# Kernel optimization log

Measured on AMD Instinct MI355X. Metric: run time of the kernel, lower is better.

Reference implementation:

```python
import jax, jax.numpy as jnp
import numpy as np

N, M, D, E, G = 2048, 1024, 1024, 64, 16  # queries, keys, feat_dim, embed_dim, groups


def setup_inputs() -> dict:
    key = jax.random.key(0)
    ks = jax.random.split(key, 8)
    s = 0.02
    return {
        "ref_feat": jax.random.normal(ks[0], (N, D), jnp.float32),
        "sup_feat": jax.random.normal(ks[1], (M, D), jnp.float32),
        "position_embedding": jax.random.normal(ks[2], (1, E, N, M), jnp.float32),
        "fc_w": jax.random.normal(ks[3], (D, D), jnp.float32) * s,
        "fc_b": jnp.zeros((D,), jnp.float32),
        "wg_w": jax.random.normal(ks[4], (G, E, 1, 1), jnp.float32) * s,
        "wg_b": jnp.zeros((G,), jnp.float32),
        "wq_w": jax.random.normal(ks[5], (D, D), jnp.float32) * s,
        "wq_b": jnp.zeros((D,), jnp.float32),
        "wk_w": jax.random.normal(ks[6], (D, D), jnp.float32) * s,
        "wk_b": jnp.zeros((D,), jnp.float32),
        "wv_w": jax.random.normal(ks[7], (D, D, 1, 1), jnp.float32) * 0.01,
        "wv_b": jnp.zeros((D,), jnp.float32),
    }


def reference(ref_feat, sup_feat, position_embedding, fc_w, fc_b, wg_w, wg_b,
              wq_w, wq_b, wk_w, wk_b, wv_w, wv_b):
    n, d = ref_feat.shape
    g = wg_w.shape[0]
    dg = d // g  # head dim

    # shared fc (layer 0) with relu on both streams
    sup = jax.nn.relu(sup_feat @ fc_w.T + fc_b)   # [M, D]
    ref = jax.nn.relu(ref_feat @ fc_w.T + fc_b)   # [N, D]

    # position bias: 1x1 conv (E->G) + relu -> [N, G, M]
    aff_weight = jax.nn.relu(
        jnp.einsum('ge,enm->ngm', wg_w[:, :, 0, 0], position_embedding[0])
        + wg_b[None, :, None])

    # per-head q/k
    q = (ref @ wq_w.T + wq_b).reshape(n, g, dg)          # [N, G, dg]
    k = (sup @ wk_w.T + wk_b).reshape(-1, g, dg)          # [M, G, dg]

    aff_scale = jnp.einsum('ngd,mgd->ngm', q, k) / jnp.sqrt(jnp.float32(dg))
    weighted_aff = jnp.log(aff_weight + 1e-6) + aff_scale  # [N, G, M]
    aff_softmax = jax.nn.softmax(weighted_aff, axis=2)

    # value aggregation: v = sup, then grouped 1x1 conv Wv
    out_t = jnp.einsum('ngm,md->ngd', aff_softmax, sup)   # [N, G, D]
    wv = wv_w[:, :, 0, 0].reshape(g, dg, d)               # [G, D/G out, D in per group]
    attention = jnp.einsum('ngc,gjc->ngj', out_t, wv).reshape(n, d) + wv_b

    return ref + attention
```

## Files before the change

kernel.cpp:

```cpp
#include <hip/hip_runtime.h>

typedef __attribute__((ext_vector_type(8))) short short8;
typedef __attribute__((ext_vector_type(4))) float f32x4;

__device__ __forceinline__ unsigned short bf16r(float f) {
  unsigned int u = __float_as_uint(f);
  u = (u + 0x7FFFu + ((u >> 16) & 1u)) >> 16;
  return (unsigned short)u;
}
__device__ __forceinline__ float bf2f(unsigned short h) {
  return __uint_as_float(((unsigned int)h) << 16);
}
__device__ __forceinline__ unsigned int pk2(float a, float b) {
  return (unsigned int)bf16r(a) | ((unsigned int)bf16r(b) << 16);
}

__device__ __forceinline__ void gload16(const unsigned short* g, unsigned short* l) {
  __builtin_amdgcn_global_load_lds(
      (const __attribute__((address_space(1))) unsigned int*)g,
      (__attribute__((address_space(3))) unsigned int*)l, 16, 0, 0);
}

__device__ __forceinline__ void stage_tile(const unsigned short* __restrict__ gsrc, int ld,
                                           int k0, unsigned short* Ls, int t) {
  const int w = t >> 6;
  const int o0 = t * 16;
  const int r0 = o0 >> 6;
  const int c0 = ((((o0 >> 4) & 3) ^ ((r0 >> 2) & 3)) << 3);
  const int r1 = r0 + 64;
  const int c1 = ((((o0 >> 4) & 3) ^ ((r1 >> 2) & 3)) << 3);
  gload16(gsrc + (long)r0 * ld + k0 + c0, Ls + w * 512);
  gload16(gsrc + (long)r1 * ld + k0 + c1, Ls + 2048 + w * 512);
}

__device__ __forceinline__ void kloop(const unsigned short* __restrict__ A,
                                      const unsigned short* __restrict__ B,
                                      int lda, int ldb, int K,
                                      unsigned short* As, unsigned short* Bs,
                                      int t, f32x4 acc[4][4]) {
  const int lane = t & 63;
  const int w = t >> 6;
  const int wr = w >> 1, wc = w & 1;
  const int ra = lane & 15;
  const int ch = ((lane >> 4) ^ (ra >> 2)) << 3;
  stage_tile(A, lda, 0, As, t);
  stage_tile(B, ldb, 0, Bs, t);
  __syncthreads();
  for (int k0 = 0; k0 < K; k0 += 32) {
    const int p = (k0 >> 5) & 1;
    unsigned short* Ac = As + p * 4096;
    unsigned short* Bc = Bs + p * 4096;
    if (k0 + 32 < K) {
      stage_tile(A, lda, k0 + 32, As + (p ^ 1) * 4096, t);
      stage_tile(B, ldb, k0 + 32, Bs + (p ^ 1) * 4096, t);
    }
    short8 a[4], b[4];
#pragma unroll
    for (int i = 0; i < 4; ++i)
      a[i] = *(const short8*)(Ac + (wr * 64 + i * 16 + ra) * 32 + ch);
#pragma unroll
    for (int j = 0; j < 4; ++j)
      b[j] = *(const short8*)(Bc + (wc * 64 + j * 16 + ra) * 32 + ch);
#pragma unroll
    for (int i = 0; i < 4; ++i)
#pragma unroll
      for (int j = 0; j < 4; ++j)
        acc[i][j] = __builtin_amdgcn_mfma_f32_16x16x32_bf16(b[j], a[i], acc[i][j], 0, 0, 0);
    __syncthreads();
  }
}

__global__ __launch_bounds__(256)
void cvt_all(const float* __restrict__ ref, const float* __restrict__ sup,
             const float* __restrict__ fcw, const float* __restrict__ wq,
             const float* __restrict__ wk, const float* __restrict__ wv,
             unsigned short* __restrict__ Xb, unsigned short* __restrict__ FCW,
             unsigned short* __restrict__ WQB, unsigned short* __restrict__ WKB,
             unsigned short* __restrict__ WVB) {
  long u = ((long)blockIdx.x * 256 + threadIdx.x) * 4;
  const float* src; unsigned short* dst;
  if (u < 2097152)      { src = ref + u;             dst = Xb + u; }
  else if (u < 3145728) { src = sup + (u - 2097152); dst = Xb + u; }
  else if (u < 4194304) { src = fcw + (u - 3145728); dst = FCW + (u - 3145728); }
  else if (u < 5242880) { src = wq + (u - 4194304);  dst = WQB + (u - 4194304); }
  else if (u < 6291456) { src = wk + (u - 5242880);  dst = WKB + (u - 5242880); }
  else                  { src = wv + (u - 6291456);  dst = WVB + (u - 6291456); }
  float4 v = *(const float4*)src;
  ushort4 o;
  o.x = bf16r(v.x); o.y = bf16r(v.y); o.z = bf16r(v.z); o.w = bf16r(v.w);
  *(ushort4*)dst = o;
}

__global__ __launch_bounds__(256)
void gemm_fc(const unsigned short* __restrict__ X, const unsigned short* __restrict__ W,
             const float* __restrict__ bias, unsigned short* __restrict__ RS) {
  __shared__ unsigned short As[8192], Bs[8192];
  const int t = threadIdx.x, lane = t & 63, w = t >> 6;
  const int wr = w >> 1, wc = w & 1;
  const int row0 = blockIdx.x * 128, col0 = blockIdx.y * 128;
  f32x4 acc[4][4] = {};
  kloop(X + (long)row0 * 1024, W + (long)col0 * 1024, 1024, 1024, 1024, As, Bs, t, acc);
  const int rl = lane & 15, q4 = (lane >> 4) << 2;
#pragma unroll
  for (int i = 0; i < 4; ++i) {
    int rr = row0 + wr * 64 + i * 16 + rl;
#pragma unroll
    for (int j = 0; j < 4; ++j) {
      int cc = col0 + wc * 64 + j * 16 + q4;
      float4 bb = *(const float4*)(bias + cc);
      float v0 = fmaxf(acc[i][j][0] + bb.x, 0.f);
      float v1 = fmaxf(acc[i][j][1] + bb.y, 0.f);
      float v2 = fmaxf(acc[i][j][2] + bb.z, 0.f);
      float v3 = fmaxf(acc[i][j][3] + bb.w, 0.f);
      uint2 o; o.x = pk2(v0, v1); o.y = pk2(v2, v3);
      *(uint2*)(RS + (long)rr * 1024 + cc) = o;
    }
  }
}

__global__ __launch_bounds__(256)
void gemm_qkv(const unsigned short* __restrict__ RS,
              const unsigned short* __restrict__ WQ, const unsigned short* __restrict__ WK,
              const unsigned short* __restrict__ WV,
              const float* __restrict__ qb, const float* __restrict__ kb,
              unsigned short* __restrict__ QG, unsigned short* __restrict__ KG,
              unsigned short* __restrict__ SVT) {
  const int z = blockIdx.z;
  const unsigned short* A; const unsigned short* B; int M;
  if (z == 0)      { A = RS;           B = WQ; M = 2048; }
  else if (z == 1) { A = RS + 2097152; B = WK; M = 1024; }
  else             { A = RS + 2097152; B = WV; M = 1024; }
  const int row0 = blockIdx.x * 128;
  if (row0 >= M) return;
  const int col0 = blockIdx.y * 128;
  __shared__ unsigned short As[8192], Bs[8192];
  const int t = threadIdx.x, lane = t & 63, w = t >> 6;
  const int wr = w >> 1, wc = w & 1;
  f32x4 acc[4][4] = {};
  kloop(A + (long)row0 * 1024, B + (long)col0 * 1024, 1024, 1024, 1024, As, Bs, t, acc);
  const int rl = lane & 15, q4 = (lane >> 4) << 2;
  if (z == 2) {
#pragma unroll
    for (int i = 0; i < 4; ++i) {
      int rr = row0 + wr * 64 + i * 16 + rl;
#pragma unroll
      for (int j = 0; j < 4; ++j) {
        int cg = col0 + wc * 64 + j * 16 + q4;
#pragma unroll
        for (int ri = 0; ri < 4; ++ri) {
          int gg = (cg + ri) >> 6, jj = (cg + ri) & 63;
          SVT[(long)gg * 65536 + (long)jj * 1024 + rr] = bf16r(acc[i][j][ri]);
        }
      }
    }
  } else {
    const float* bias = z ? kb : qb;
    unsigned short* out = z ? KG : QG;
    const long gs = z ? 65536 : 131072;
#pragma unroll
    for (int i = 0; i < 4; ++i) {
      int rr = row0 + wr * 64 + i * 16 + rl;
#pragma unroll
      for (int j = 0; j < 4; ++j) {
        int cc = col0 + wc * 64 + j * 16 + q4;
        float4 bb = *(const float4*)(bias + cc);
        int gg = cc >> 6, jj = cc & 63;
        uint2 o;
        o.x = pk2(acc[i][j][0] + bb.x, acc[i][j][1] + bb.y);
        o.y = pk2(acc[i][j][2] + bb.z, acc[i][j][3] + bb.w);
        *(uint2*)(out + (long)gg * gs + (long)rr * 64 + jj) = o;
      }
    }
  }
}

__global__ __launch_bounds__(512)
void pe_attn2(const float* __restrict__ pe, const float* __restrict__ wgw,
              const float* __restrict__ wgb,
              const unsigned short* __restrict__ QG,
              const unsigned short* __restrict__ KG,
              const unsigned short* __restrict__ SVT,
              float* __restrict__ Opart, float* __restrict__ ms)
{
  __shared__ __align__(16) unsigned char peb[2][16384];
  __shared__ __align__(16) unsigned char Ps[8][2048];
  __shared__ float wgs[1024];

  const int t = threadIdx.x;
  const int lane = t & 63;
  const int w = t >> 6;
  const int n0 = blockIdx.x * 16;
  const int sp = blockIdx.y;
  const int mbase = sp * 256;
  const int rl = lane & 15;
  const int hi = lane >> 4;
  const int g0 = w * 2;
  const float C2 = 0.18033688011112042f;

  for (int i = t; i < 1024; i += 512) wgs[(i & 63) * 16 + (i >> 6)] = wgw[i];

  short8 qf0k0 = *(const short8*)(QG + (long)g0 * 131072 + (long)(n0 + rl) * 64 + hi * 8);
  short8 qf0k1 = *(const short8*)(QG + (long)g0 * 131072 + (long)(n0 + rl) * 64 + 32 + hi * 8);
  short8 qf1k0 = *(const short8*)(QG + (long)(g0 + 1) * 131072 + (long)(n0 + rl) * 64 + hi * 8);
  short8 qf1k1 = *(const short8*)(QG + (long)(g0 + 1) * 131072 + (long)(n0 + rl) * 64 + 32 + hi * 8);

  auto STAGE = [&](int cg2) {
    const int buf = cg2 & 1;
    const int e = (cg2 & 15) * 4 + (w >> 1);
    const int m0s = mbase + (cg2 >> 4) * 64;
#pragma unroll
    for (int q = 0; q < 2; ++q) {
      int r = (w & 1) * 8 + q * 4 + hi;
      gload16((const unsigned short*)(pe + (long)e * 2097152 + (long)(n0 + r) * 1024 +
                                      m0s + 4 * ((lane & 15) ^ (r & 7))),
              (unsigned short*)(&peb[buf][(w >> 1) * 4096 + ((w & 1) * 8 + q * 4) * 256 + lane * 16]));
    }
  };

  STAGE(0);

  f32x4 Oa[2][4] = {};
  float mx0 = -1e30f, mx1 = -1e30f, sm0 = 0.f, sm1 = 0.f;
  const float bias0 = wgb[g0], bias1 = wgb[g0 + 1];
  unsigned char* Pw = Ps[w];
  const int qmsk = (rl & 7) << 4;

  int cg = 0;
  for (int chunk = 0; chunk < 4; ++chunk) {
    const int m0c = mbase + chunk * 64;
    f32x4 conv[2][4];
#pragma unroll
    for (int mb = 0; mb < 4; ++mb) {
      conv[0][mb] = (f32x4){bias0, bias0, bias0, bias0};
      conv[1][mb] = (f32x4){bias1, bias1, bias1, bias1};
    }
    for (int grp = 0; grp < 16; ++grp, ++cg) {
      __syncthreads();
      if (cg + 1 < 64) STAGE(cg + 1);
      const unsigned char* pb = peb[cg & 1];
      const int ebase = (cg & 15) * 4;
#pragma unroll
      for (int ii = 0; ii < 4; ++ii) {
        float wg0 = wgs[(ebase + ii) * 16 + g0];
        float wg1 = wgs[(ebase + ii) * 16 + g0 + 1];
#pragma unroll
        for (int mb = 0; mb < 4; ++mb) {
          f32x4 p = *(const f32x4*)(pb + ii * 4096 + rl * 256 + ((mb * 64 + hi * 16) ^ qmsk));
          conv[0][mb] += p * wg0;
          conv[1][mb] += p * wg1;
        }
      }
    }
    f32x4 sa[2][4];
#pragma unroll
    for (int mb = 0; mb < 4; ++mb) {
      const long krow = (long)(m0c + mb * 16 + rl) * 64 + hi * 8;
      short8 kf0a = *(const short8*)(KG + (long)g0 * 65536 + krow);
      short8 kf0b = *(const short8*)(KG + (long)g0 * 65536 + krow + 32);
      short8 kf1a = *(const short8*)(KG + (long)(g0 + 1) * 65536 + krow);
      short8 kf1b = *(const short8*)(KG + (long)(g0 + 1) * 65536 + krow + 32);
      f32x4 z0 = {}, z1 = {};
      z0 = __builtin_amdgcn_mfma_f32_16x16x32_bf16(kf0a, qf0k0, z0, 0, 0, 0);
      z0 = __builtin_amdgcn_mfma_f32_16x16x32_bf16(kf0b, qf0k1, z0, 0, 0, 0);
      z1 = __builtin_amdgcn_mfma_f32_16x16x32_bf16(kf1a, qf1k0, z1, 0, 0, 0);
      z1 = __builtin_amdgcn_mfma_f32_16x16x32_bf16(kf1b, qf1k1, z1, 0, 0, 0);
      sa[0][mb] = z0;
      sa[1][mb] = z1;
    }
#pragma unroll
    for (int gi = 0; gi < 2; ++gi) {
      const int g = g0 + gi;
      float wv[4][4];
      float cmax = -1e30f;
#pragma unroll
      for (int mb = 0; mb < 4; ++mb)
#pragma unroll
        for (int ri = 0; ri < 4; ++ri) {
          float v = __builtin_amdgcn_logf(fmaxf(conv[gi][mb][ri], 0.f) + 1e-6f)
                  + sa[gi][mb][ri] * C2;
          wv[mb][ri] = v;
          cmax = fmaxf(cmax, v);
        }
      cmax = fmaxf(cmax, __shfl_xor(cmax, 16));
      cmax = fmaxf(cmax, __shfl_xor(cmax, 32));
      float oldm = gi ? mx1 : mx0;
      float newm = fmaxf(oldm, cmax);
      float scale = __builtin_amdgcn_exp2f(oldm - newm);
      float csum = 0.f;
      float pv[4][4];
#pragma unroll
      for (int mb = 0; mb < 4; ++mb)
#pragma unroll
        for (int ri = 0; ri < 4; ++ri) {
          float p = __builtin_amdgcn_exp2f(wv[mb][ri] - newm);
          pv[mb][ri] = p;
          csum += p;
        }
      csum += __shfl_xor(csum, 16);
      csum += __shfl_xor(csum, 32);
      if (gi) { mx1 = newm; sm1 = sm1 * scale + csum; }
      else    { mx0 = newm; sm0 = sm0 * scale + csum; }
#pragma unroll
      for (int jb = 0; jb < 4; ++jb) Oa[gi][jb] *= scale;
#pragma unroll
      for (int mb = 0; mb < 4; ++mb) {
        uint2 o;
        o.x = pk2(pv[mb][0], pv[mb][1]);
        o.y = pk2(pv[mb][2], pv[mb][3]);
        *(uint2*)(Pw + ((rl * 128 + mb * 32 + hi * 8) ^ qmsk)) = o;
      }
#pragma unroll
      for (int jb = 0; jb < 4; ++jb) {
#pragma unroll
        for (int mc = 0; mc < 2; ++mc) {
          short8 sv = *(const short8*)(SVT + (long)g * 65536 +
                                       (long)(jb * 16 + rl) * 1024 + m0c + mc * 32 + hi * 8);
          short8 pf = *(const short8*)(Pw + ((rl * 128 + mc * 64 + hi * 16) ^ qmsk));
          Oa[gi][jb] = __builtin_amdgcn_mfma_f32_16x16x32_bf16(sv, pf, Oa[gi][jb], 0, 0, 0);
        }
      }
    }
  }
  const int n = n0 + rl;
#pragma unroll
  for (int gi = 0; gi < 2; ++gi) {
    if (hi == 0) {
      float2 v; v.x = gi ? mx1 : mx0; v.y = gi ? sm1 : sm0;
      *(float2*)(ms + (((long)sp * 2048 + n) * 16 + g0 + gi) * 2) = v;
    }
#pragma unroll
    for (int jb = 0; jb < 4; ++jb) {
      *(f32x4*)(Opart + ((long)sp * 2048 + n) * 1024 + (g0 + gi) * 64 + jb * 16 + hi * 4) =
          Oa[gi][jb];
    }
  }
}

__global__ __launch_bounds__(256)
void combine(const float* __restrict__ Opart, const float* __restrict__ ms,
             const unsigned short* __restrict__ RS, const float* __restrict__ wvb,
             float* __restrict__ out) {
  const int n = blockIdx.x;
  const int t = threadIdx.x;
  const int g = t >> 4;
  float mv0, mv1, mv2, mv3, sv0, sv1, sv2, sv3;
  {
    float2 a = *(const float2*)(ms + (((long)0 * 2048 + n) * 16 + g) * 2);
    float2 b = *(const float2*)(ms + (((long)1 * 2048 + n) * 16 + g) * 2);
    float2 c = *(const float2*)(ms + (((long)2 * 2048 + n) * 16 + g) * 2);
    float2 d = *(const float2*)(ms + (((long)3 * 2048 + n) * 16 + g) * 2);
    mv0 = a.x; sv0 = a.y; mv1 = b.x; sv1 = b.y;
    mv2 = c.x; sv2 = c.y; mv3 = d.x; sv3 = d.y;
  }
  float M = fmaxf(fmaxf(mv0, mv1), fmaxf(mv2, mv3));
  float w0 = __builtin_amdgcn_exp2f(mv0 - M);
  float w1 = __builtin_amdgcn_exp2f(mv1 - M);
  float w2 = __builtin_amdgcn_exp2f(mv2 - M);
  float w3 = __builtin_amdgcn_exp2f(mv3 - M);
  float S = sv0 * w0 + sv1 * w1 + sv2 * w2 + sv3 * w3;
  f32x4 acc;
  acc  = (*(const f32x4*)(Opart + ((long)0 * 2048 + n) * 1024 + t * 4)) * w0;
  acc += (*(const f32x4*)(Opart + ((long)1 * 2048 + n) * 1024 + t * 4)) * w1;
  acc += (*(const f32x4*)(Opart + ((long)2 * 2048 + n) * 1024 + t * 4)) * w2;
  acc += (*(const f32x4*)(Opart + ((long)3 * 2048 + n) * 1024 + t * 4)) * w3;
  float rs = __builtin_amdgcn_rcpf(S);
  const int oc = t * 4;
  float4 wb = *(const float4*)(wvb + oc);
  ushort4 r4 = *(const ushort4*)(RS + (long)n * 1024 + oc);
  float4 o;
  o.x = acc[0] * rs + wb.x + bf2f(r4.x);
  o.y = acc[1] * rs + wb.y + bf2f(r4.y);
  o.z = acc[2] * rs + wb.z + bf2f(r4.z);
  o.w = acc[3] * rs + wb.w + bf2f(r4.w);
  *(float4*)(out + (long)n * 1024 + oc) = o;
}

extern "C" void kernel_launch(void* const* d_in, const int* in_sizes, int n_in,
                              void* d_out, int out_size, void* d_ws, size_t ws_size,
                              hipStream_t stream) {
  const float* ref_feat = (const float*)d_in[0];
  const float* sup_feat = (const float*)d_in[1];
  const float* pe       = (const float*)d_in[2];
  const float* fc_w     = (const float*)d_in[3];
  const float* fc_b     = (const float*)d_in[4];
  const float* wg_w     = (const float*)d_in[5];
  const float* wg_b     = (const float*)d_in[6];
  const float* wq_w     = (const float*)d_in[7];
  const float* wq_b     = (const float*)d_in[8];
  const float* wk_w     = (const float*)d_in[9];
  const float* wk_b     = (const float*)d_in[10];
  const float* wv_w     = (const float*)d_in[11];
  const float* wv_b     = (const float*)d_in[12];

  char* ws = (char*)d_ws;
  unsigned short* Xb  = (unsigned short*)(ws);
  unsigned short* FCW = (unsigned short*)(ws + 6291456);
  unsigned short* WQB = (unsigned short*)(ws + 8388608);
  unsigned short* WKB = (unsigned short*)(ws + 10485760);
  unsigned short* WVB = (unsigned short*)(ws + 12582912);
  unsigned short* RS  = (unsigned short*)(ws + 14680064);
  unsigned short* QG  = (unsigned short*)(ws + 20971520);
  unsigned short* KG  = (unsigned short*)(ws + 25165824);
  unsigned short* SVT = (unsigned short*)(ws + 27262976);
  float*          Opart = (float*)(ws + 29360128);
  float*          msb   = (float*)(ws + 62914560);

  cvt_all<<<7168, 256, 0, stream>>>(ref_feat, sup_feat, fc_w, wq_w, wk_w, wv_w,
                                    Xb, FCW, WQB, WKB, WVB);
  gemm_fc<<<dim3(24, 8), 256, 0, stream>>>(Xb, FCW, fc_b, RS);
  gemm_qkv<<<dim3(16, 8, 3), 256, 0, stream>>>(RS, WQB, WKB, WVB, wq_b, wk_b, QG, KG, SVT);
  pe_attn2<<<dim3(128, 4), 512, 0, stream>>>(pe, wg_w, wg_b, QG, KG, SVT, Opart, msb);
  combine<<<2048, 256, 0, stream>>>(Opart, msb, RS, wv_b, (float*)d_out);
}
```

Before: 301.5 us.

## Stream position embedding directly from global memory and halve key splits

The attention kernel stops staging the position-embedding tensor through double-buffered LDS with async global-to-LDS loads. Each thread now reads its own pe vectors straight from global memory into registers and does the 1x1 conv there, then hands the conv result through a swizzled per-wave LDS scratch to the MFMA fragment layout. The key split drops from 4 to 2, so each block covers 512 keys, and the combine kernel only merges two partials, which cuts partial-output traffic. The softmax scale C2 is folded into Q at the projection epilogue. The risks are fewer blocks (256 instead of 512) and loss of the async-copy overlap, which leaves the pe stream dependent on plain vector global loads for latency hiding.

```diff
diff --git a/kernel.cpp b/kernel.cpp
--- a/kernel.cpp
+++ b/kernel.cpp
@@ -157,6 +157,7 @@
     const float* bias = z ? kb : qb;
     unsigned short* out = z ? KG : QG;
     const long gs = z ? 65536 : 131072;
+    const float scl = z ? 1.0f : 0.18033688011112042f;
 #pragma unroll
     for (int i = 0; i < 4; ++i) {
       int rr = row0 + wr * 64 + i * 16 + rl;
@@ -166,8 +167,8 @@
         float4 bb = *(const float4*)(bias + cc);
         int gg = cc >> 6, jj = cc & 63;
         uint2 o;
-        o.x = pk2(acc[i][j][0] + bb.x, acc[i][j][1] + bb.y);
-        o.y = pk2(acc[i][j][2] + bb.z, acc[i][j][3] + bb.w);
+        o.x = pk2((acc[i][j][0] + bb.x) * scl, (acc[i][j][1] + bb.y) * scl);
+        o.y = pk2((acc[i][j][2] + bb.z) * scl, (acc[i][j][3] + bb.w) * scl);
         *(uint2*)(out + (long)gg * gs + (long)rr * 64 + jj) = o;
       }
     }
@@ -175,112 +176,88 @@
 }
 
 __global__ __launch_bounds__(512)
-void pe_attn2(const float* __restrict__ pe, const float* __restrict__ wgw,
+void pe_attn3(const float* __restrict__ pe, const float* __restrict__ wgw,
               const float* __restrict__ wgb,
               const unsigned short* __restrict__ QG,
               const unsigned short* __restrict__ KG,
               const unsigned short* __restrict__ SVT,
               float* __restrict__ Opart, float* __restrict__ ms)
 {
-  __shared__ __align__(16) unsigned char peb[2][16384];
+  __shared__ float wgs[1024];
+  __shared__ __align__(16) float Lw[8][1024];
   __shared__ __align__(16) unsigned char Ps[8][2048];
-  __shared__ float wgs[1024];
 
   const int t = threadIdx.x;
   const int lane = t & 63;
   const int w = t >> 6;
+  const int rl = lane & 15;
+  const int hi = lane >> 4;
   const int n0 = blockIdx.x * 16;
   const int sp = blockIdx.y;
-  const int mbase = sp * 256;
-  const int rl = lane & 15;
-  const int hi = lane >> 4;
   const int g0 = w * 2;
-  const float C2 = 0.18033688011112042f;
 
   for (int i = t; i < 1024; i += 512) wgs[(i & 63) * 16 + (i >> 6)] = wgw[i];
+  __syncthreads();
 
   short8 qf0k0 = *(const short8*)(QG + (long)g0 * 131072 + (long)(n0 + rl) * 64 + hi * 8);
   short8 qf0k1 = *(const short8*)(QG + (long)g0 * 131072 + (long)(n0 + rl) * 64 + 32 + hi * 8);
   short8 qf1k0 = *(const short8*)(QG + (long)(g0 + 1) * 131072 + (long)(n0 + rl) * 64 + hi * 8);
   short8 qf1k1 = *(const short8*)(QG + (long)(g0 + 1) * 131072 + (long)(n0 + rl) * 64 + 32 + hi * 8);
 
-  auto STAGE = [&](int cg2) {
-    const int buf = cg2 & 1;
-    const int e = (cg2 & 15) * 4 + (w >> 1);
-    const int m0s = mbase + (cg2 >> 4) * 64;
-#pragma unroll
-    for (int q = 0; q < 2; ++q) {
-      int r = (w & 1) * 8 + q * 4 + hi;
-      gload16((const unsigned short*)(pe + (long)e * 2097152 + (long)(n0 + r) * 1024 +
-                                      m0s + 4 * ((lane & 15) ^ (r & 7))),
-              (unsigned short*)(&peb[buf][(w >> 1) * 4096 + ((w & 1) * 8 + q * 4) * 256 + lane * 16]));
-    }
-  };
-
-  STAGE(0);
-
   f32x4 Oa[2][4] = {};
   float mx0 = -1e30f, mx1 = -1e30f, sm0 = 0.f, sm1 = 0.f;
   const float bias0 = wgb[g0], bias1 = wgb[g0 + 1];
+  float* Lww = Lw[w];
   unsigned char* Pw = Ps[w];
   const int qmsk = (rl & 7) << 4;
-
-  int cg = 0;
-  for (int chunk = 0; chunk < 4; ++chunk) {
-    const int m0c = mbase + chunk * 64;
-    f32x4 conv[2][4];
-#pragma unroll
-    for (int mb = 0; mb < 4; ++mb) {
-      conv[0][mb] = (f32x4){bias0, bias0, bias0, bias0};
-      conv[1][mb] = (f32x4){bias1, bias1, bias1, bias1};
-    }
-    for (int grp = 0; grp < 16; ++grp, ++cg) {
-      __syncthreads();
-      if (cg + 1 < 64) STAGE(cg + 1);
-      const unsigned char* pb = peb[cg & 1];
-      const int ebase = (cg & 15) * 4;
-#pragma unroll
-      for (int ii = 0; ii < 4; ++ii) {
-        float wg0 = wgs[(ebase + ii) * 16 + g0];
-        float wg1 = wgs[(ebase + ii) * 16 + g0 + 1];
-#pragma unroll
-        for (int mb = 0; mb < 4; ++mb) {
-          f32x4 p = *(const f32x4*)(pb + ii * 4096 + rl * 256 + ((mb * 64 + hi * 16) ^ qmsk));
-          conv[0][mb] += p * wg0;
-          conv[1][mb] += p * wg1;
-        }
-      }
-    }
-    f32x4 sa[2][4];
-#pragma unroll
-    for (int mb = 0; mb < 4; ++mb) {
-      const long krow = (long)(m0c + mb * 16 + rl) * 64 + hi * 8;
-      short8 kf0a = *(const short8*)(KG + (long)g0 * 65536 + krow);
-      short8 kf0b = *(const short8*)(KG + (long)g0 * 65536 + krow + 32);
-      short8 kf1a = *(const short8*)(KG + (long)(g0 + 1) * 65536 + krow);
-      short8 kf1b = *(const short8*)(KG + (long)(g0 + 1) * 65536 + krow + 32);
-      f32x4 z0 = {}, z1 = {};
-      z0 = __builtin_amdgcn_mfma_f32_16x16x32_bf16(kf0a, qf0k0, z0, 0, 0, 0);
-      z0 = __builtin_amdgcn_mfma_f32_16x16x32_bf16(kf0b, qf0k1, z0, 0, 0, 0);
-      z1 = __builtin_amdgcn_mfma_f32_16x16x32_bf16(kf1a, qf1k0, z1, 0, 0, 0);
-      z1 = __builtin_amdgcn_mfma_f32_16x16x32_bf16(kf1b, qf1k1, z1, 0, 0, 0);
-      sa[0][mb] = z0;
-      sa[1][mb] = z1;
+  const int rx = rl & 7;
+
+  for (int chunk = 0; chunk < 8; ++chunk) {
+    const int m0c = sp * 512 + chunk * 64;
+    f32x4 c0[4], c1[4];
+#pragma unroll
+    for (int q = 0; q < 4; ++q) {
+      c0[q] = (f32x4){bias0, bias0, bias0, bias0};
+      c1[q] = (f32x4){bias1, bias1, bias1, bias1};
+    }
+    const float* pb = pe + (long)(n0 + rl) * 1024 + m0c + hi * 16;
+#pragma unroll 2
+    for (int e = 0; e < 64; ++e) {
+      const f32x4* ps = (const f32x4*)(pb + (long)e * 2097152);
+      f32x4 p0 = ps[0], p1 = ps[1], p2 = ps[2], p3 = ps[3];
+      float2 wg2 = *(const float2*)(wgs + e * 16 + g0);
+      c0[0] += p0 * wg2.x; c0[1] += p1 * wg2.x; c0[2] += p2 * wg2.x; c0[3] += p3 * wg2.x;
+      c1[0] += p0 * wg2.y; c1[1] += p1 * wg2.y; c1[2] += p2 * wg2.y; c1[3] += p3 * wg2.y;
     }
 #pragma unroll
     for (int gi = 0; gi < 2; ++gi) {
       const int g = g0 + gi;
+#pragma unroll
+      for (int q = 0; q < 4; ++q)
+        *(f32x4*)(Lww + rl * 64 + ((((hi << 2) + q) ^ rx) << 2)) = gi ? c1[q] : c0[q];
+      f32x4 sa[4];
+#pragma unroll
+      for (int mb = 0; mb < 4; ++mb) {
+        const long krow = (long)g * 65536 + (long)(m0c + mb * 16 + rl) * 64 + hi * 8;
+        short8 ka = *(const short8*)(KG + krow);
+        short8 kb2 = *(const short8*)(KG + krow + 32);
+        f32x4 z = {};
+        z = __builtin_amdgcn_mfma_f32_16x16x32_bf16(ka, gi ? qf1k0 : qf0k0, z, 0, 0, 0);
+        z = __builtin_amdgcn_mfma_f32_16x16x32_bf16(kb2, gi ? qf1k1 : qf0k1, z, 0, 0, 0);
+        sa[mb] = z;
+      }
       float wv[4][4];
       float cmax = -1e30f;
 #pragma unroll
-      for (int mb = 0; mb < 4; ++mb)
+      for (int mb = 0; mb < 4; ++mb) {
+        f32x4 cv = *(const f32x4*)(Lww + rl * 64 + ((((mb << 2) + hi) ^ rx) << 2));
 #pragma unroll
         for (int ri = 0; ri < 4; ++ri) {
-          float v = __builtin_amdgcn_logf(fmaxf(conv[gi][mb][ri], 0.f) + 1e-6f)
-                  + sa[gi][mb][ri] * C2;
+          float v = __builtin_amdgcn_logf(fmaxf(cv[ri], 0.f) + 1e-6f) + sa[mb][ri];
           wv[mb][ri] = v;
           cmax = fmaxf(cmax, v);
         }
+      }
       cmax = fmaxf(cmax, __shfl_xor(cmax, 16));
       cmax = fmaxf(cmax, __shfl_xor(cmax, 32));
       float oldm = gi ? mx1 : mx0;
@@ -343,26 +320,15 @@
   const int n = blockIdx.x;
   const int t = threadIdx.x;
   const int g = t >> 4;
-  float mv0, mv1, mv2, mv3, sv0, sv1, sv2, sv3;
-  {
-    float2 a = *(const float2*)(ms + (((long)0 * 2048 + n) * 16 + g) * 2);
-    float2 b = *(const float2*)(ms + (((long)1 * 2048 + n) * 16 + g) * 2);
-    float2 c = *(const float2*)(ms + (((long)2 * 2048 + n) * 16 + g) * 2);
-    float2 d = *(const float2*)(ms + (((long)3 * 2048 + n) * 16 + g) * 2);
-    mv0 = a.x; sv0 = a.y; mv1 = b.x; sv1 = b.y;
-    mv2 = c.x; sv2 = c.y; mv3 = d.x; sv3 = d.y;
-  }
-  float M = fmaxf(fmaxf(mv0, mv1), fmaxf(mv2, mv3));
-  float w0 = __builtin_amdgcn_exp2f(mv0 - M);
-  float w1 = __builtin_amdgcn_exp2f(mv1 - M);
-  float w2 = __builtin_amdgcn_exp2f(mv2 - M);
-  float w3 = __builtin_amdgcn_exp2f(mv3 - M);
-  float S = sv0 * w0 + sv1 * w1 + sv2 * w2 + sv3 * w3;
+  float2 a = *(const float2*)(ms + ((long)n * 16 + g) * 2);
+  float2 b = *(const float2*)(ms + (((long)2048 + n) * 16 + g) * 2);
+  float M = fmaxf(a.x, b.x);
+  float w0 = __builtin_amdgcn_exp2f(a.x - M);
+  float w1 = __builtin_amdgcn_exp2f(b.x - M);
+  float S = a.y * w0 + b.y * w1;
   f32x4 acc;
-  acc  = (*(const f32x4*)(Opart + ((long)0 * 2048 + n) * 1024 + t * 4)) * w0;
-  acc += (*(const f32x4*)(Opart + ((long)1 * 2048 + n) * 1024 + t * 4)) * w1;
-  acc += (*(const f32x4*)(Opart + ((long)2 * 2048 + n) * 1024 + t * 4)) * w2;
-  acc += (*(const f32x4*)(Opart + ((long)3 * 2048 + n) * 1024 + t * 4)) * w3;
+  acc  = (*(const f32x4*)(Opart + (long)n * 1024 + t * 4)) * w0;
+  acc += (*(const f32x4*)(Opart + ((long)2048 + n) * 1024 + t * 4)) * w1;
   float rs = __builtin_amdgcn_rcpf(S);
   const int oc = t * 4;
   float4 wb = *(const float4*)(wvb + oc);
@@ -403,12 +369,12 @@
   unsigned short* KG  = (unsigned short*)(ws + 25165824);
   unsigned short* SVT = (unsigned short*)(ws + 27262976);
   float*          Opart = (float*)(ws + 29360128);
-  float*          msb   = (float*)(ws + 62914560);
+  float*          msb   = (float*)(ws + 46137344);
 
   cvt_all<<<7168, 256, 0, stream>>>(ref_feat, sup_feat, fc_w, wq_w, wk_w, wv_w,
                                     Xb, FCW, WQB, WKB, WVB);
   gemm_fc<<<dim3(24, 8), 256, 0, stream>>>(Xb, FCW, fc_b, RS);
   gemm_qkv<<<dim3(16, 8, 3), 256, 0, stream>>>(RS, WQB, WKB, WVB, wq_b, wk_b, QG, KG, SVT);
-  pe_attn2<<<dim3(128, 4), 512, 0, stream>>>(pe, wg_w, wg_b, QG, KG, SVT, Opart, msb);
+  pe_attn3<<<dim3(128, 2), 512, 0, stream>>>(pe, wg_w, wg_b, QG, KG, SVT, Opart, msb);
   combine<<<2048, 256, 0, stream>>>(Opart, msb, RS, wv_b, (float*)d_out);
 }
```

After: 588.3 us. +95.1%, slower.
